# Performance work log

Hardware: AMD Instinct MI355X
Metric: run time of the kernel (lower is better)

Reference implementation:

```python
import jax, jax.numpy as jnp
import numpy as np

HT_H, HT_W = 512, 512          # Hough accumulator grid
SPHERE_SIZE = 32768            # Gaussian-sphere bins
NUM_VOTES = 1_500_000          # rows in vote_mapping
BATCH, CHANNEL = 2, 64         # channel % 4 == 0 required by the module


def setup_inputs() -> dict:
    key = jax.random.key(0)
    k1, k2, k3, k4 = jax.random.split(key, 4)
    x = jax.random.normal(k1, (BATCH, CHANNEL, HT_H, HT_W), dtype=jnp.float32)
    ht_idx = jax.random.randint(k2, (NUM_VOTES,), 0, HT_H * HT_W, dtype=jnp.int32)
    sphere_idx = jax.random.randint(k3, (NUM_VOTES,), 0, SPHERE_SIZE, dtype=jnp.int32)
    weight = jax.random.uniform(k4, (NUM_VOTES,), dtype=jnp.float32)
    return {"x": x, "ht_idx": ht_idx, "sphere_idx": sphere_idx, "weight": weight}


def reference(x, ht_idx, sphere_idx, weight):
    b, c, h, w = x.shape
    # SPHERE_CUDA.forward: split channels into 4 groups, flatten HT grid
    xf = x.reshape(b * 4, c // 4, h * w)              # [B4, C4, HW]
    # HT2SPHERE: gather each vote's HT cell, scale by vote weight,
    # scatter-add into its sphere bin.
    votes = xf[:, :, ht_idx] * weight                  # [B4, C4, V]
    out = jax.ops.segment_sum(
        jnp.moveaxis(votes, -1, 0), sphere_idx, num_segments=SPHERE_SIZE
    )                                                  # [S, B4, C4]
    out = jnp.moveaxis(out, 0, -1)                     # [B4, C4, S]
    return out.reshape(b, c, SPHERE_SIZE)              # [B, C, S]
```

## Files before the change

kernel.cpp:

```cpp
#include <hip/hip_runtime.h>
#include <stdint.h>


#define S_BINS   32768
#define NBUCKET  1024
#define BINS     32
#define CAP      2048
#define CHUNK    4096
#define HT_BITS  18

__device__ __forceinline__ unsigned bf16_rne(float f) {
    unsigned u = __float_as_uint(f);
    return (u + 0x7FFFu + ((u >> 16) & 1u)) >> 16;
}

__global__ void transpose_x_bf16_kernel(const float* __restrict__ x,
                                        uint32_t* __restrict__ xTb, int HW) {
    __shared__ float tile[64][129];
    const int ht0 = blockIdx.x * 64;
    const int tid = threadIdx.x;
    for (int e = tid; e < 128 * 64; e += 256) {
        const int ch = e >> 6, hl = e & 63;
        tile[hl][ch] = x[(size_t)ch * HW + ht0 + hl];
    }
    __syncthreads();
    for (int e = tid; e < 64 * 64; e += 256) {
        const int hl = e >> 6, cp = e & 63;
        const unsigned lo = bf16_rne(tile[hl][cp]);
        const unsigned hi = bf16_rne(tile[hl][cp + 64]);
        xTb[(size_t)(ht0 + hl) * 64 + cp] = lo | (hi << 16);
    }
}

__global__ void init_kernel(int* __restrict__ cursor, int* __restrict__ spillCnt) {
    const int t = threadIdx.x;
    cursor[t] = t * CAP;
    if (t == 0) *spillCnt = 0;
}

__global__ __launch_bounds__(512) void reorder_kernel(
    const int* __restrict__ ht, const int* __restrict__ sp,
    const float* __restrict__ w, int* __restrict__ cursor,
    uint2* __restrict__ records, uint2* __restrict__ spillRec,
    int* __restrict__ spillBkt, int* __restrict__ spillCnt, int V) {
    __shared__ uint2 rec[CHUNK];
    __shared__ uint16_t bid[CHUNK];
    __shared__ int hist[NBUCKET], start[NBUCKET], cur[NBUCKET], gbase[NBUCKET];
    __shared__ int psum[512];
    const int blk = blockIdx.x, t = threadIdx.x;
    const int base = blk * CHUNK, end = min(V, base + CHUNK), n = end - base;
    hist[2 * t] = 0; hist[2 * t + 1] = 0;
    __syncthreads();
    for (int v = base + t; v < end; v += 512) atomicAdd(&hist[sp[v] >> 5], 1);
    __syncthreads();
    const int l0 = hist[2 * t], l1 = hist[2 * t + 1];
    psum[t] = l0 + l1;
    __syncthreads();
    for (int off = 1; off < 512; off <<= 1) {
        const int add = (t >= off) ? psum[t - off] : 0;
        __syncthreads();
        psum[t] += add;
        __syncthreads();
    }
    int run = (t == 0) ? 0 : psum[t - 1];
    start[2 * t]     = run; cur[2 * t]     = run; run += l0;
    start[2 * t + 1] = run; cur[2 * t + 1] = run;
    if (l0) gbase[2 * t]     = atomicAdd(&cursor[2 * t],     l0);
    if (l1) gbase[2 * t + 1] = atomicAdd(&cursor[2 * t + 1], l1);
    __syncthreads();
    for (int v = base + t; v < end; v += 512) {
        const int s = sp[v];
        const int b = s >> 5, sl = s & 31;
        const int pos = atomicAdd(&cur[b], 1);
        rec[pos] = make_uint2((unsigned)ht[v] | ((unsigned)sl << HT_BITS),
                              __float_as_uint(w[v]));
        bid[pos] = (uint16_t)b;
    }
    __syncthreads();
    for (int i = t; i < n; i += 512) {
        const int b = bid[i];
        const int slot = gbase[b] + (i - start[b]);
        if (slot < (b + 1) * CAP) {
            records[slot] = rec[i];
        } else {
            const int pos = atomicAdd(spillCnt, 1);
            spillRec[pos] = rec[i];
            spillBkt[pos] = b;
        }
    }
}

__global__ __launch_bounds__(512) void accum_kernel(
    const uint32_t* __restrict__ xTb, const uint2* __restrict__ records,
    const int* __restrict__ cursor, float* __restrict__ out) {
    __shared__ uint2 sorted[CAP];
    __shared__ __align__(16) char rawbuf[BINS * 129 * 4];
    __shared__ int hist[BINS], off[BINS + 1], cur[BINS];
    uint2* raw = (uint2*)rawbuf;
    const uint2* xTb2 = (const uint2*)xTb;
    const int bkt = blockIdx.x, t = threadIdx.x;
    const int lane = t & 63, wv = t >> 6;
    const int half = lane >> 5, hl = lane & 31;
    const int n = min(cursor[bkt] - bkt * CAP, CAP);
    const int rbase = bkt * CAP;
    float a[4][4];
#pragma unroll
    for (int i = 0; i < 4; ++i)
#pragma unroll
        for (int j = 0; j < 4; ++j) a[i][j] = 0.f;

    if (t < BINS) hist[t] = 0;
    __syncthreads();
    for (int i = t; i < n; i += 512) {
        const uint2 r = records[rbase + i];
        raw[i] = r;
        atomicAdd(&hist[(r.x >> HT_BITS) & 31], 1);
    }
    __syncthreads();
    if (t == 0) {
        int run = 0;
        for (int j = 0; j < BINS; ++j) { off[j] = run; cur[j] = run; run += hist[j]; }
        off[BINS] = run;
    }
    __syncthreads();
    for (int i = t; i < n; i += 512) {
        const uint2 r = raw[i];
        const int pos = atomicAdd(&cur[(r.x >> HT_BITS) & 31], 1);
        sorted[pos] = r;
    }
    __syncthreads();
#pragma unroll
    for (int bb = 0; bb < 4; ++bb) {
        const int f = wv * 4 + bb;
        const int s0 = off[f], s1 = off[f + 1];
        for (int k = s0; k < s1; k += 16) {
#pragma unroll
            for (int u = 0; u < 8; ++u) {
                const int kk = k + 2 * u + half;
                if (kk < s1) {
                    const uint2 r = sorted[kk];
                    const uint2 g = xTb2[(size_t)(r.x & 0x3FFFF) * 32 + hl];
                    const float wt = __uint_as_float(r.y);
                    a[bb][0] += __uint_as_float(g.x << 16) * wt;
                    a[bb][1] += __uint_as_float(g.x & 0xFFFF0000u) * wt;
                    a[bb][2] += __uint_as_float(g.y << 16) * wt;
                    a[bb][3] += __uint_as_float(g.y & 0xFFFF0000u) * wt;
                }
            }
        }
    }
#pragma unroll
    for (int bb = 0; bb < 4; ++bb)
#pragma unroll
        for (int j = 0; j < 4; ++j)
            a[bb][j] += __shfl_xor(a[bb][j], 32);
    __syncthreads();
    float* epi = (float*)rawbuf;
    if (half == 0) {
#pragma unroll
        for (int bb = 0; bb < 4; ++bb) {
            const int f = wv * 4 + bb;
            epi[f * 129 + 2 * hl]      = a[bb][0];
            epi[f * 129 + 2 * hl + 64] = a[bb][1];
            epi[f * 129 + 2 * hl + 1]  = a[bb][2];
            epi[f * 129 + 2 * hl + 65] = a[bb][3];
        }
    }
    __syncthreads();
    for (int i = t; i < 128 * BINS; i += 512) {
        const int ch = i >> 5, bin = i & 31;
        out[(size_t)ch * S_BINS + bkt * BINS + bin] = epi[bin * 129 + ch];
    }
}

__global__ void spill_kernel(const uint32_t* __restrict__ xTb,
                             const uint2* __restrict__ spillRec,
                             const int* __restrict__ spillBkt,
                             const int* __restrict__ spillCnt,
                             float* __restrict__ out) {
    const int cnt = *spillCnt;
    const long total = (long)cnt * 64;
    for (long u = (long)blockIdx.x * blockDim.x + threadIdx.x; u < total;
         u += (long)gridDim.x * blockDim.x) {
        const int i  = (int)(u >> 6);
        const int cp = (int)(u & 63);
        const uint2 r = spillRec[i];
        const int s = (spillBkt[i] << 5) | ((r.x >> HT_BITS) & 31);
        const uint32_t g = xTb[(size_t)(r.x & 0x3FFFF) * 64 + cp];
        const float wt = __uint_as_float(r.y);
        atomicAdd(&out[(size_t)cp * S_BINS + s],
                  __uint_as_float(g << 16) * wt);
        atomicAdd(&out[(size_t)(cp + 64) * S_BINS + s],
                  __uint_as_float(g & 0xFFFF0000u) * wt);
    }
}

__global__ void direct_kernel(const float* __restrict__ x,
                              const int* __restrict__ ht_idx,
                              const int* __restrict__ sp_idx,
                              const float* __restrict__ weight,
                              float* __restrict__ out, int V, int HW, int S,
                              int CH) {
    const int v = blockIdx.x * 2 + (threadIdx.x >> 7);
    if (v >= V) return;
    const int ch = threadIdx.x & 127;
    if (ch >= CH) return;
    atomicAdd(&out[(size_t)ch * S + sp_idx[v]],
              x[(size_t)ch * HW + ht_idx[v]] * weight[v]);
}

extern "C" void kernel_launch(void* const* d_in, const int* in_sizes, int n_in,
                              void* d_out, int out_size, void* d_ws, size_t ws_size,
                              hipStream_t stream) {
    const float* x  = (const float*)d_in[0];
    const int*   ht = (const int*)d_in[1];
    const int*   sp = (const int*)d_in[2];
    const float* w  = (const float*)d_in[3];
    float* out = (float*)d_out;

    const int HW = 512 * 512;
    const int CH = in_sizes[0] / HW;
    const int S  = out_size / CH;
    const int V  = in_sizes[1];
    const int nblk = (V + CHUNK - 1) / CHUNK;

    const size_t xTb_bytes = (size_t)CH * HW * sizeof(uint16_t);
    const size_t rec_bytes = (size_t)NBUCKET * CAP * sizeof(uint2);
    const size_t spr_bytes = (size_t)V * sizeof(uint2);
    const size_t spb_bytes = (size_t)V * sizeof(int);
    const size_t cur_bytes = (size_t)NBUCKET * sizeof(int);
    const size_t cnt_bytes = 64;
    const size_t need = xTb_bytes + rec_bytes + spr_bytes + spb_bytes +
                        cur_bytes + cnt_bytes;

    if (CH == 128 && S == S_BINS && HW == (1 << HT_BITS) && ws_size >= need) {
        char* p = (char*)d_ws;
        uint32_t* xTb  = (uint32_t*)p;  p += xTb_bytes;
        uint2* records = (uint2*)p;     p += rec_bytes;
        uint2* spillRec= (uint2*)p;     p += spr_bytes;
        int* spillBkt  = (int*)p;       p += spb_bytes;
        int* cursor    = (int*)p;       p += cur_bytes;
        int* spillCnt  = (int*)p;

        init_kernel<<<1, NBUCKET, 0, stream>>>(cursor, spillCnt);
        transpose_x_bf16_kernel<<<HW / 64, 256, 0, stream>>>(x, xTb, HW);
        reorder_kernel<<<nblk, 512, 0, stream>>>(ht, sp, w, cursor, records,
                                                 spillRec, spillBkt, spillCnt, V);
        accum_kernel<<<NBUCKET, 512, 0, stream>>>(xTb, records, cursor, out);
        spill_kernel<<<256, 256, 0, stream>>>(xTb, spillRec, spillBkt, spillCnt,
                                              out);
    } else {
        hipMemsetAsync(out, 0, (size_t)out_size * sizeof(float), stream);
        direct_kernel<<<(V + 1) / 2, 256, 0, stream>>>(x, ht, sp, w, out, V, HW,
                                                       S, CH);
    }
}
```

Before: 317.7 us.

## Fuse transpose and reorder into one launch, widen accum gathers to 16 bytes

The bf16 transpose and the vote bucketing now run as one kernel whose block index picks the role, and the init kernel becomes a memset with cursors made relative to each bucket. This removes two launches and lets the transpose overlap with the reorder. The accumulate kernel now gathers uint4 per lane, with four records per wavefront instead of two, and adds an extra shuffle stage to reduce across them. In exchange the fused kernel uses the larger reorder shared-memory footprint for every block, and the accumulate kernel needs more registers.

After: 327.8 us. 3.2% more time.

```diff
diff --git a/kernel.cpp b/kernel.cpp
--- a/kernel.cpp
+++ b/kernel.cpp
@@ -8,46 +8,49 @@
 #define CAP      2048
 #define CHUNK    4096
 #define HT_BITS  18
+#define SMEM_BYTES (CHUNK*8 + CHUNK*2 + 4*NBUCKET*4 + 512*4)
 
 __device__ __forceinline__ unsigned bf16_rne(float f) {
     unsigned u = __float_as_uint(f);
     return (u + 0x7FFFu + ((u >> 16) & 1u)) >> 16;
 }
 
-__global__ void transpose_x_bf16_kernel(const float* __restrict__ x,
-                                        uint32_t* __restrict__ xTb, int HW) {
-    __shared__ float tile[64][129];
-    const int ht0 = blockIdx.x * 64;
-    const int tid = threadIdx.x;
-    for (int e = tid; e < 128 * 64; e += 256) {
-        const int ch = e >> 6, hl = e & 63;
-        tile[hl][ch] = x[(size_t)ch * HW + ht0 + hl];
-    }
-    __syncthreads();
-    for (int e = tid; e < 64 * 64; e += 256) {
-        const int hl = e >> 6, cp = e & 63;
-        const unsigned lo = bf16_rne(tile[hl][cp]);
-        const unsigned hi = bf16_rne(tile[hl][cp + 64]);
-        xTb[(size_t)(ht0 + hl) * 64 + cp] = lo | (hi << 16);
-    }
-}
-
-__global__ void init_kernel(int* __restrict__ cursor, int* __restrict__ spillCnt) {
+__global__ __launch_bounds__(512) void prep_kernel(
+    const float* __restrict__ x, const int* __restrict__ ht,
+    const int* __restrict__ sp, const float* __restrict__ w,
+    uint32_t* __restrict__ xTb, int* __restrict__ cursor,
+    uint2* __restrict__ records, uint2* __restrict__ spillRec,
+    int* __restrict__ spillBkt, int* __restrict__ spillCnt,
+    int V, int HW, int TBLK) {
+    __shared__ __align__(16) char smem[SMEM_BYTES];
     const int t = threadIdx.x;
-    cursor[t] = t * CAP;
-    if (t == 0) *spillCnt = 0;
-}
-
-__global__ __launch_bounds__(512) void reorder_kernel(
-    const int* __restrict__ ht, const int* __restrict__ sp,
-    const float* __restrict__ w, int* __restrict__ cursor,
-    uint2* __restrict__ records, uint2* __restrict__ spillRec,
-    int* __restrict__ spillBkt, int* __restrict__ spillCnt, int V) {
-    __shared__ uint2 rec[CHUNK];
-    __shared__ uint16_t bid[CHUNK];
-    __shared__ int hist[NBUCKET], start[NBUCKET], cur[NBUCKET], gbase[NBUCKET];
-    __shared__ int psum[512];
-    const int blk = blockIdx.x, t = threadIdx.x;
+    if ((int)blockIdx.x < TBLK) {
+        float* tile = (float*)smem;
+        const int ht0 = blockIdx.x * 64;
+        const float2* x2 = (const float2*)x;
+        for (int e = t; e < 128 * 32; e += 512) {
+            const int ch = e >> 5, hp = e & 31;
+            const float2 v = x2[((size_t)ch * HW + ht0) / 2 + hp];
+            tile[(2 * hp) * 129 + ch]     = v.x;
+            tile[(2 * hp + 1) * 129 + ch] = v.y;
+        }
+        __syncthreads();
+        for (int e = t; e < 64 * 64; e += 512) {
+            const int hl = e >> 6, cp = e & 63;
+            const unsigned lo = bf16_rne(tile[hl * 129 + cp]);
+            const unsigned hi = bf16_rne(tile[hl * 129 + cp + 64]);
+            xTb[(size_t)(ht0 + hl) * 64 + cp] = lo | (hi << 16);
+        }
+        return;
+    }
+    uint2*    rec    = (uint2*)smem;
+    uint16_t* bid    = (uint16_t*)(smem + CHUNK * 8);
+    int* hist   = (int*)(smem + CHUNK * 8 + CHUNK * 2);
+    int* startB = hist + NBUCKET;
+    int* curB   = startB + NBUCKET;
+    int* gbase  = curB + NBUCKET;
+    int* psum   = gbase + NBUCKET;
+    const int blk = blockIdx.x - TBLK;
     const int base = blk * CHUNK, end = min(V, base + CHUNK), n = end - base;
     hist[2 * t] = 0; hist[2 * t + 1] = 0;
     __syncthreads();
@@ -63,15 +66,15 @@
         __syncthreads();
     }
     int run = (t == 0) ? 0 : psum[t - 1];
-    start[2 * t]     = run; cur[2 * t]     = run; run += l0;
-    start[2 * t + 1] = run; cur[2 * t + 1] = run;
+    startB[2 * t]     = run; curB[2 * t]     = run; run += l0;
+    startB[2 * t + 1] = run; curB[2 * t + 1] = run;
     if (l0) gbase[2 * t]     = atomicAdd(&cursor[2 * t],     l0);
     if (l1) gbase[2 * t + 1] = atomicAdd(&cursor[2 * t + 1], l1);
     __syncthreads();
     for (int v = base + t; v < end; v += 512) {
         const int s = sp[v];
         const int b = s >> 5, sl = s & 31;
-        const int pos = atomicAdd(&cur[b], 1);
+        const int pos = atomicAdd(&curB[b], 1);
         rec[pos] = make_uint2((unsigned)ht[v] | ((unsigned)sl << HT_BITS),
                               __float_as_uint(w[v]));
         bid[pos] = (uint16_t)b;
@@ -79,9 +82,9 @@
     __syncthreads();
     for (int i = t; i < n; i += 512) {
         const int b = bid[i];
-        const int slot = gbase[b] + (i - start[b]);
-        if (slot < (b + 1) * CAP) {
-            records[slot] = rec[i];
+        const int slot = gbase[b] + (i - startB[b]);
+        if (slot < CAP) {
+            records[(size_t)b * CAP + slot] = rec[i];
         } else {
             const int pos = atomicAdd(spillCnt, 1);
             spillRec[pos] = rec[i];
@@ -97,17 +100,17 @@
     __shared__ __align__(16) char rawbuf[BINS * 129 * 4];
     __shared__ int hist[BINS], off[BINS + 1], cur[BINS];
     uint2* raw = (uint2*)rawbuf;
-    const uint2* xTb2 = (const uint2*)xTb;
+    const uint4* xTb4 = (const uint4*)xTb;
     const int bkt = blockIdx.x, t = threadIdx.x;
     const int lane = t & 63, wv = t >> 6;
-    const int half = lane >> 5, hl = lane & 31;
-    const int n = min(cursor[bkt] - bkt * CAP, CAP);
+    const int q = lane >> 4, ql = lane & 15;
+    const int n = min(cursor[bkt], CAP);
     const int rbase = bkt * CAP;
-    float a[4][4];
+    float a[4][8];
 #pragma unroll
     for (int i = 0; i < 4; ++i)
 #pragma unroll
-        for (int j = 0; j < 4; ++j) a[i][j] = 0.f;
+        for (int j = 0; j < 8; ++j) a[i][j] = 0.f;
 
     if (t < BINS) hist[t] = 0;
     __syncthreads();
@@ -133,18 +136,22 @@
     for (int bb = 0; bb < 4; ++bb) {
         const int f = wv * 4 + bb;
         const int s0 = off[f], s1 = off[f + 1];
-        for (int k = s0; k < s1; k += 16) {
+        for (int k = s0; k < s1; k += 32) {
 #pragma unroll
             for (int u = 0; u < 8; ++u) {
-                const int kk = k + 2 * u + half;
+                const int kk = k + 4 * u + q;
                 if (kk < s1) {
                     const uint2 r = sorted[kk];
-                    const uint2 g = xTb2[(size_t)(r.x & 0x3FFFF) * 32 + hl];
+                    const uint4 g = xTb4[(size_t)(r.x & 0x3FFFF) * 16 + ql];
                     const float wt = __uint_as_float(r.y);
                     a[bb][0] += __uint_as_float(g.x << 16) * wt;
-                    a[bb][1] += __uint_as_float(g.x & 0xFFFF0000u) * wt;
-                    a[bb][2] += __uint_as_float(g.y << 16) * wt;
-                    a[bb][3] += __uint_as_float(g.y & 0xFFFF0000u) * wt;
+                    a[bb][4] += __uint_as_float(g.x & 0xFFFF0000u) * wt;
+                    a[bb][1] += __uint_as_float(g.y << 16) * wt;
+                    a[bb][5] += __uint_as_float(g.y & 0xFFFF0000u) * wt;
+                    a[bb][2] += __uint_as_float(g.z << 16) * wt;
+                    a[bb][6] += __uint_as_float(g.z & 0xFFFF0000u) * wt;
+                    a[bb][3] += __uint_as_float(g.w << 16) * wt;
+                    a[bb][7] += __uint_as_float(g.w & 0xFFFF0000u) * wt;
                 }
             }
         }
@@ -152,18 +159,21 @@
 #pragma unroll
     for (int bb = 0; bb < 4; ++bb)
 #pragma unroll
-        for (int j = 0; j < 4; ++j)
+        for (int j = 0; j < 8; ++j) {
+            a[bb][j] += __shfl_xor(a[bb][j], 16);
             a[bb][j] += __shfl_xor(a[bb][j], 32);
+        }
     __syncthreads();
     float* epi = (float*)rawbuf;
-    if (half == 0) {
+    if (q == 0) {
 #pragma unroll
         for (int bb = 0; bb < 4; ++bb) {
             const int f = wv * 4 + bb;
-            epi[f * 129 + 2 * hl]      = a[bb][0];
-            epi[f * 129 + 2 * hl + 64] = a[bb][1];
-            epi[f * 129 + 2 * hl + 1]  = a[bb][2];
-            epi[f * 129 + 2 * hl + 65] = a[bb][3];
+#pragma unroll
+            for (int i = 0; i < 4; ++i) {
+                epi[f * 129 + 4 * ql + i]      = a[bb][i];
+                epi[f * 129 + 4 * ql + 64 + i] = a[bb][4 + i];
+            }
         }
     }
     __syncthreads();
@@ -223,6 +233,7 @@
     const int S  = out_size / CH;
     const int V  = in_sizes[1];
     const int nblk = (V + CHUNK - 1) / CHUNK;
+    const int TBLK = HW / 64;
 
     const size_t xTb_bytes = (size_t)CH * HW * sizeof(uint16_t);
     const size_t rec_bytes = (size_t)NBUCKET * CAP * sizeof(uint2);
@@ -242,10 +253,10 @@
         int* cursor    = (int*)p;       p += cur_bytes;
         int* spillCnt  = (int*)p;
 
-        init_kernel<<<1, NBUCKET, 0, stream>>>(cursor, spillCnt);
-        transpose_x_bf16_kernel<<<HW / 64, 256, 0, stream>>>(x, xTb, HW);
-        reorder_kernel<<<nblk, 512, 0, stream>>>(ht, sp, w, cursor, records,
-                                                 spillRec, spillBkt, spillCnt, V);
+        hipMemsetAsync(cursor, 0, cur_bytes + sizeof(int), stream);
+        prep_kernel<<<TBLK + nblk, 512, 0, stream>>>(
+            x, ht, sp, w, xTb, cursor, records, spillRec, spillBkt, spillCnt,
+            V, HW, TBLK);
         accum_kernel<<<NBUCKET, 512, 0, stream>>>(xTb, records, cursor, out);
         spill_kernel<<<256, 256, 0, stream>>>(xTb, spillRec, spillBkt, spillCnt,
                                               out);
```
